# Kernel tuning notes

Measured on AMD Instinct MI355X. Metric: run time of the kernel, lower is better.

## Reference

```python
import jax, jax.numpy as jnp
import numpy as np

N_NODES, FEAT, EMB, BATCH, NUM_SAMPLE = 100000, 256, 256, 10000, 32


def setup_inputs() -> dict:
    key = jax.random.key(0)
    ks = jax.random.split(key, 8)
    sc = 1.0 / np.sqrt(FEAT).astype(np.float32)
    return {
        "nodes": jax.random.randint(ks[0], (BATCH,), 0, N_NODES),
        "neigh_idx": jax.random.randint(ks[1], (BATCH, NUM_SAMPLE), 0, N_NODES),
        "id2feat": jax.random.normal(ks[2], (N_NODES, FEAT), jnp.float32),
        "Wq": jax.random.normal(ks[3], (FEAT, EMB), jnp.float32) * sc,
        "bq": jnp.zeros((EMB,), jnp.float32),
        "Wk": jax.random.normal(ks[4], (FEAT, EMB), jnp.float32) * sc,
        "bk": jnp.zeros((EMB,), jnp.float32),
        "Wv": jax.random.normal(ks[5], (FEAT, EMB), jnp.float32) * sc,
        "bv": jnp.zeros((EMB,), jnp.float32),
    }


def reference(nodes, neigh_idx, id2feat, Wq, bq, Wk, bk, Wv, bv):
    # Gather: self feats [B, F] and sampled neighbor feats [B, S, F]
    self_feats = id2feat[nodes]
    neigh_feats = id2feat[neigh_idx]
    S = neigh_idx.shape[1]
    # Keys/values over [neighbors, self] -> [B, S+1, F]
    cat = jnp.concatenate([neigh_feats, self_feats[:, None, :]], axis=1)
    Q = self_feats @ Wq + bq               # [B, E]
    K = cat @ Wk + bk                       # [B, S+1, E]
    V = cat @ Wv + bv                       # [B, S+1, E]
    scores = jnp.einsum('be,bse->bs', Q, K)  # [B, S+1]
    # Faithful to original mask loop: with full neighbor lists, columns >= num_sample
    # (the appended self key) are masked out.
    mask = jnp.arange(S + 1) >= S
    scores = jnp.where(mask[None, :], -jnp.inf, scores)
    attn = jax.nn.softmax(scores, axis=-1)   # [B, S+1]
    return jnp.einsum('bs,bse->be', attn, V)  # [B, E]
```

## Files before the change

kernel.cpp:

```cpp
#include <hip/hip_runtime.h>
#include <math.h>

#define F 256
#define E 256
#define S 32
#define CH 4
#define LDK 40

typedef __attribute__((ext_vector_type(8))) short short8;
typedef __attribute__((ext_vector_type(4))) float f32x4;

__device__ __forceinline__ ushort f2bf(float x) {
    uint u = __float_as_uint(x);
    return (ushort)((u + 0x7fffu + ((u >> 16) & 1u)) >> 16);
}
__device__ __forceinline__ float bf2f(ushort h) {
    return __uint_as_float(((uint)h) << 16);
}
__device__ __forceinline__ void split4(const float* x, uint2& ph, uint2& pl) {
    ushort h[4], l[4];
#pragma unroll
    for (int i = 0; i < 4; ++i) { h[i] = f2bf(x[i]); l[i] = f2bf(x[i] - bf2f(h[i])); }
    ph.x = (uint)h[0] | ((uint)h[1] << 16); ph.y = (uint)h[2] | ((uint)h[3] << 16);
    pl.x = (uint)l[0] | ((uint)l[1] << 16); pl.y = (uint)l[2] | ((uint)l[3] << 16);
}
__device__ __forceinline__ uint4 pack8(const ushort* h) {
    uint4 r;
    r.x = (uint)h[0] | ((uint)h[1] << 16); r.y = (uint)h[2] | ((uint)h[3] << 16);
    r.z = (uint)h[4] | ((uint)h[5] << 16); r.w = (uint)h[6] | ((uint)h[7] << 16);
    return r;
}

template<bool INSPLIT, bool OUTSPLIT>
__global__ __launch_bounds__(512) void mfma_gemm(const float* __restrict__ X,
                                                 const int* __restrict__ idx,
                                                 const ushort* __restrict__ BTh,
                                                 const ushort* __restrict__ BTl,
                                                 const float* __restrict__ Bf,
                                                 const float* __restrict__ bias,
                                                 float* __restrict__ out,
                                                 ushort* __restrict__ outh,
                                                 ushort* __restrict__ outl,
                                                 int rows) {
    __shared__ ushort Ah[64][LDK], Al[64][LDK];
    __shared__ ushort Bh[256][LDK], Bl[256][LDK];

    const int tid = threadIdx.x;
    const int lane = tid & 63, wave = tid >> 6;
    const int wm = wave >> 2, wn = wave & 3;
    const int fr = lane & 15, fk = lane >> 4;
    const int row0 = blockIdx.x * 64;

    const int arL = tid >> 3;
    const int akL = (tid & 7) * 4;
    const int ar = row0 + arL;
    const int arc = ar < rows ? ar : rows - 1;
    const long arow = idx ? (long)idx[arc] : (long)arc;
    const float* aptr = X + arow * (long)F + akL;

    const int bcol = tid & 255;
    const int bkh = (tid >> 8) * 16;

    f32x4 acc[2][4];
#pragma unroll
    for (int m = 0; m < 2; ++m)
#pragma unroll
        for (int n = 0; n < 4; ++n) acc[m][n] = (f32x4){0.f, 0.f, 0.f, 0.f};

    for (int k0 = 0; k0 < F; k0 += 32) {
        const float4 av = *reinterpret_cast<const float4*>(&aptr[k0]);
        uint2 ah, al;
        split4(&av.x, ah, al);

        uint4 wh0, wh1, wl0, wl1;
        if constexpr (INSPLIT) {
            const float* bp = Bf + (size_t)bcol * F + k0 + bkh;
            float4 b0 = *reinterpret_cast<const float4*>(bp);
            float4 b1 = *reinterpret_cast<const float4*>(bp + 4);
            float4 b2 = *reinterpret_cast<const float4*>(bp + 8);
            float4 b3 = *reinterpret_cast<const float4*>(bp + 12);
            uint2 h0, l0, h1, l1, h2, l2, h3, l3;
            split4(&b0.x, h0, l0); split4(&b1.x, h1, l1);
            split4(&b2.x, h2, l2); split4(&b3.x, h3, l3);
            wh0 = make_uint4(h0.x, h0.y, h1.x, h1.y);
            wh1 = make_uint4(h2.x, h2.y, h3.x, h3.y);
            wl0 = make_uint4(l0.x, l0.y, l1.x, l1.y);
            wl1 = make_uint4(l2.x, l2.y, l3.x, l3.y);
        } else {
            const ushort* bph = BTh + (size_t)bcol * F + k0 + bkh;
            const ushort* bpl = BTl + (size_t)bcol * F + k0 + bkh;
            wh0 = *reinterpret_cast<const uint4*>(bph);
            wh1 = *reinterpret_cast<const uint4*>(bph + 8);
            wl0 = *reinterpret_cast<const uint4*>(bpl);
            wl1 = *reinterpret_cast<const uint4*>(bpl + 8);
        }

        __syncthreads();
        *reinterpret_cast<uint2*>(&Ah[arL][akL]) = ah;
        *reinterpret_cast<uint2*>(&Al[arL][akL]) = al;
        *reinterpret_cast<uint4*>(&Bh[bcol][bkh]) = wh0;
        *reinterpret_cast<uint4*>(&Bh[bcol][bkh + 8]) = wh1;
        *reinterpret_cast<uint4*>(&Bl[bcol][bkh]) = wl0;
        *reinterpret_cast<uint4*>(&Bl[bcol][bkh + 8]) = wl1;
        __syncthreads();

        short8 a_h[2], a_l[2];
#pragma unroll
        for (int m = 0; m < 2; ++m) {
            a_h[m] = *reinterpret_cast<const short8*>(&Ah[wm * 32 + m * 16 + fr][fk * 8]);
            a_l[m] = *reinterpret_cast<const short8*>(&Al[wm * 32 + m * 16 + fr][fk * 8]);
        }
#pragma unroll
        for (int n = 0; n < 4; ++n) {
            const short8 b_h = *reinterpret_cast<const short8*>(&Bh[wn * 64 + n * 16 + fr][fk * 8]);
            const short8 b_l = *reinterpret_cast<const short8*>(&Bl[wn * 64 + n * 16 + fr][fk * 8]);
#pragma unroll
            for (int m = 0; m < 2; ++m) {
                acc[m][n] = __builtin_amdgcn_mfma_f32_16x16x32_bf16(a_h[m], b_h, acc[m][n], 0, 0, 0);
                acc[m][n] = __builtin_amdgcn_mfma_f32_16x16x32_bf16(a_h[m], b_l, acc[m][n], 0, 0, 0);
                acc[m][n] = __builtin_amdgcn_mfma_f32_16x16x32_bf16(a_l[m], b_h, acc[m][n], 0, 0, 0);
            }
        }
    }

#pragma unroll
    for (int n = 0; n < 4; ++n) {
        const int col = wn * 64 + n * 16 + fr;
        float bb = 0.f;
        if constexpr (!OUTSPLIT) bb = bias[col];
#pragma unroll
        for (int m = 0; m < 2; ++m) {
#pragma unroll
            for (int r = 0; r < 4; ++r) {
                const int orow = row0 + wm * 32 + m * 16 + fk * 4 + r;
                if (orow < rows) {
                    if constexpr (OUTSPLIT) {
                        const float v = acc[m][n][r];
                        const ushort h = f2bf(v);
                        outh[(size_t)orow * F + col] = h;
                        outl[(size_t)orow * F + col] = f2bf(v - bf2f(h));
                    } else {
                        out[(size_t)orow * E + col] = acc[m][n][r] + bb;
                    }
                }
            }
        }
    }
}

__global__ __launch_bounds__(256) void prep_misc(const float* __restrict__ Wk,
                                                 const float* __restrict__ bq,
                                                 const float* __restrict__ Wv,
                                                 float* __restrict__ c,
                                                 ushort* __restrict__ WvTh,
                                                 ushort* __restrict__ WvTl) {
    if (blockIdx.x < 4) {
        __shared__ float bqs[F];
        bqs[threadIdx.x] = bq[threadIdx.x];
        __syncthreads();
        const int lane = threadIdx.x & 63, w = threadIdx.x >> 6;
        const float4 b4 = *reinterpret_cast<const float4*>(&bqs[lane * 4]);
#pragma unroll
        for (int i = 0; i < 16; ++i) {
            const int j = blockIdx.x * 64 + w * 16 + i;
            const float4 k4 = *reinterpret_cast<const float4*>(&Wk[(size_t)j * F + lane * 4]);
            float p = k4.x * b4.x + k4.y * b4.y + k4.z * b4.z + k4.w * b4.w;
#pragma unroll
            for (int off = 32; off; off >>= 1) p += __shfl_xor(p, off);
            if (lane == 0) c[j] = p;
        }
    } else {
        __shared__ float t[64][65];
        const int tb = blockIdx.x - 4;
        const int jt = (tb & 3) * 64, kt = (tb >> 2) * 64;
        const int lk = threadIdx.x >> 2;
        const int lj = (threadIdx.x & 3) * 16;
#pragma unroll
        for (int u = 0; u < 16; u += 4) {
            const float4 v = *reinterpret_cast<const float4*>(&Wv[(size_t)(kt + lk) * E + jt + lj + u]);
            t[lk][lj + u] = v.x; t[lk][lj + u + 1] = v.y;
            t[lk][lj + u + 2] = v.z; t[lk][lj + u + 3] = v.w;
        }
        __syncthreads();
        const int oj = threadIdx.x >> 2;
        const int ok = (threadIdx.x & 3) * 16;
        ushort h[16], l[16];
#pragma unroll
        for (int u = 0; u < 16; ++u) {
            const float v = t[ok + u][oj];
            h[u] = f2bf(v); l[u] = f2bf(v - bf2f(h[u]));
        }
        ushort* ph = &WvTh[(size_t)(jt + oj) * F + kt + ok];
        ushort* pl = &WvTl[(size_t)(jt + oj) * F + kt + ok];
        *reinterpret_cast<uint4*>(ph) = pack8(h);
        *reinterpret_cast<uint4*>(ph + 8) = pack8(h + 8);
        *reinterpret_cast<uint4*>(pl) = pack8(l);
        *reinterpret_cast<uint4*>(pl + 8) = pack8(l + 8);
    }
}

__device__ __forceinline__ void ld_chunk(float4* d, int idxv, int s0,
                                         const float* __restrict__ t, int lane) {
#pragma unroll
    for (int j = 0; j < CH; ++j) {
        const int nid = __builtin_amdgcn_readlane(idxv, s0 + j);
        d[j] = *reinterpret_cast<const float4*>(&t[(size_t)nid * F + lane * 4]);
    }
}

__device__ __forceinline__ void proc_chunk(const float4* v, const float4 qv,
                                           float& m, float& l, float4& acc) {
#pragma unroll
    for (int j = 0; j < CH; ++j) {
        float p = v[j].x * qv.x + v[j].y * qv.y + v[j].z * qv.z + v[j].w * qv.w;
#pragma unroll
        for (int off = 32; off; off >>= 1) p += __shfl_xor(p, off);
        if (p <= m) {
            const float w = __expf(p - m);
            l += w;
            acc.x += w * v[j].x; acc.y += w * v[j].y;
            acc.z += w * v[j].z; acc.w += w * v[j].w;
        } else {
            const float cc = __expf(m - p);
            l = l * cc + 1.f;
            acc.x = acc.x * cc + v[j].x; acc.y = acc.y * cc + v[j].y;
            acc.z = acc.z * cc + v[j].z; acc.w = acc.w * cc + v[j].w;
            m = p;
        }
    }
}

__global__ __launch_bounds__(256) void attn_gather(const int* __restrict__ neigh_idx,
                                                   const float* __restrict__ id2feat,
                                                   float* __restrict__ qtm,
                                                   int B) {
    const int node = blockIdx.x * 4 + (threadIdx.x >> 6);
    const int lane = threadIdx.x & 63;
    if (node >= B) return;

    const int idxv = neigh_idx[node * S + (lane & (S - 1))];
    const float4 qv = *reinterpret_cast<const float4*>(&qtm[(size_t)node * F + lane * 4]);

    float m = -INFINITY, l = 0.f;
    float4 acc = make_float4(0.f, 0.f, 0.f, 0.f);

    float4 va[CH], vb[CH];
    ld_chunk(va, idxv, 0, id2feat, lane);
    ld_chunk(vb, idxv, 4, id2feat, lane);
    proc_chunk(va, qv, m, l, acc);
    ld_chunk(va, idxv, 8, id2feat, lane);
    proc_chunk(vb, qv, m, l, acc);
    ld_chunk(vb, idxv, 12, id2feat, lane);
    proc_chunk(va, qv, m, l, acc);
    ld_chunk(va, idxv, 16, id2feat, lane);
    proc_chunk(vb, qv, m, l, acc);
    ld_chunk(vb, idxv, 20, id2feat, lane);
    proc_chunk(va, qv, m, l, acc);
    ld_chunk(va, idxv, 24, id2feat, lane);
    proc_chunk(vb, qv, m, l, acc);
    ld_chunk(vb, idxv, 28, id2feat, lane);
    proc_chunk(va, qv, m, l, acc);
    proc_chunk(vb, qv, m, l, acc);

    const float inv = 1.0f / l;
    float4 o;
    o.x = acc.x * inv; o.y = acc.y * inv; o.z = acc.z * inv; o.w = acc.w * inv;
    *reinterpret_cast<float4*>(&qtm[(size_t)node * F + lane * 4]) = o;
}

extern "C" void kernel_launch(void* const* d_in, const int* in_sizes, int n_in,
                              void* d_out, int out_size, void* d_ws, size_t ws_size,
                              hipStream_t stream) {
    const int*   nodes   = (const int*)d_in[0];
    const int*   neigh   = (const int*)d_in[1];
    const float* id2feat = (const float*)d_in[2];
    const float* Wq      = (const float*)d_in[3];
    const float* bq      = (const float*)d_in[4];
    const float* Wk      = (const float*)d_in[5];
    const float* Wv      = (const float*)d_in[7];
    const float* bv      = (const float*)d_in[8];
    float* out = (float*)d_out;
    const int B = in_sizes[0];

    ushort* MT_hi  = (ushort*)d_ws;
    ushort* MT_lo  = MT_hi + 65536;
    ushort* WvT_hi = MT_lo + 65536;
    ushort* WvT_lo = WvT_hi + 65536;
    float*  cbuf   = (float*)(WvT_lo + 65536);
    float*  qtm    = cbuf + 256;

    mfma_gemm<true, true><<<dim3(4), dim3(512), 0, stream>>>(
        Wk, nullptr, nullptr, nullptr, Wq, nullptr, nullptr, MT_hi, MT_lo, 256);
    prep_misc<<<dim3(20), dim3(256), 0, stream>>>(Wk, bq, Wv, cbuf, WvT_hi, WvT_lo);
    mfma_gemm<false, false><<<dim3((B + 63) / 64), dim3(512), 0, stream>>>(
        id2feat, nodes, MT_hi, MT_lo, nullptr, cbuf, qtm, nullptr, nullptr, B);
    attn_gather<<<dim3((B + 3) / 4), dim3(256), 0, stream>>>(neigh, id2feat, qtm, B);
    mfma_gemm<false, false><<<dim3((B + 63) / 64), dim3(512), 0, stream>>>(
        qtm, nullptr, WvT_hi, WvT_lo, nullptr, bv, out, nullptr, nullptr, B);
}
```

Before: 123.0 us.

## Fuse Q projection, neighbor attention and V projection into one kernel

Merges the three per-batch kernels (Q GEMM, attention gather, V GEMM) into a single kernel that keeps the 64-row Q tile and attention output in shared memory. This drops the qtm round-trip through global memory and two launches. The weight-prep kernels are also combined into one launch, and GEMM B operands are now read straight from global memory into MFMA registers instead of being staged in LDS. In exchange, the large LDS tile (about 66KB) limits occupancy, and only 157 blocks cover the gather phase, which may reduce latency hiding for the random neighbor loads.

```diff
diff --git a/kernel.cpp b/kernel.cpp
--- a/kernel.cpp
+++ b/kernel.cpp
@@ -5,7 +5,7 @@
 #define E 256
 #define S 32
 #define CH 4
-#define LDK 40
+#define TLP 260
 
 typedef __attribute__((ext_vector_type(8))) short short8;
 typedef __attribute__((ext_vector_type(4))) float f32x4;
@@ -16,13 +16,6 @@
 }
 __device__ __forceinline__ float bf2f(ushort h) {
     return __uint_as_float(((uint)h) << 16);
-}
-__device__ __forceinline__ void split4(const float* x, uint2& ph, uint2& pl) {
-    ushort h[4], l[4];
-#pragma unroll
-    for (int i = 0; i < 4; ++i) { h[i] = f2bf(x[i]); l[i] = f2bf(x[i] - bf2f(h[i])); }
-    ph.x = (uint)h[0] | ((uint)h[1] << 16); ph.y = (uint)h[2] | ((uint)h[3] << 16);
-    pl.x = (uint)l[0] | ((uint)l[1] << 16); pl.y = (uint)l[2] | ((uint)l[3] << 16);
 }
 __device__ __forceinline__ uint4 pack8(const ushort* h) {
     uint4 r;
@@ -30,172 +23,120 @@
     r.z = (uint)h[4] | ((uint)h[5] << 16); r.w = (uint)h[6] | ((uint)h[7] << 16);
     return r;
 }
-
-template<bool INSPLIT, bool OUTSPLIT>
-__global__ __launch_bounds__(512) void mfma_gemm(const float* __restrict__ X,
-                                                 const int* __restrict__ idx,
-                                                 const ushort* __restrict__ BTh,
-                                                 const ushort* __restrict__ BTl,
-                                                 const float* __restrict__ Bf,
-                                                 const float* __restrict__ bias,
-                                                 float* __restrict__ out,
-                                                 ushort* __restrict__ outh,
-                                                 ushort* __restrict__ outl,
-                                                 int rows) {
-    __shared__ ushort Ah[64][LDK], Al[64][LDK];
-    __shared__ ushort Bh[256][LDK], Bl[256][LDK];
-
-    const int tid = threadIdx.x;
+__device__ __forceinline__ void split8(const float* x, short8& h, short8& l) {
+    ushort hh[8], ll[8];
+#pragma unroll
+    for (int i = 0; i < 8; ++i) { hh[i] = f2bf(x[i]); ll[i] = f2bf(x[i] - bf2f(hh[i])); }
+    uint4 ph = pack8(hh), pl = pack8(ll);
+    h = *reinterpret_cast<short8*>(&ph);
+    l = *reinterpret_cast<short8*>(&pl);
+}
+__device__ __forceinline__ short8 mk8(uint a, uint b, uint c, uint d) {
+    uint4 p = make_uint4(a, b, c, d);
+    return *reinterpret_cast<short8*>(&p);
+}
+__device__ __forceinline__ uint pkbf(float v) {
+    const ushort h = f2bf(v);
+    const ushort l = f2bf(v - bf2f(h));
+    return (uint)h | ((uint)l << 16);
+}
+
+__global__ __launch_bounds__(512) void prep(const float* __restrict__ Wq,
+                                            const float* __restrict__ bq,
+                                            const float* __restrict__ Wk,
+                                            const float* __restrict__ Wv,
+                                            ushort* __restrict__ MTh,
+                                            ushort* __restrict__ MTl,
+                                            ushort* __restrict__ WvTh,
+                                            ushort* __restrict__ WvTl,
+                                            float* __restrict__ c) {
+    const int blk = blockIdx.x, tid = threadIdx.x;
     const int lane = tid & 63, wave = tid >> 6;
-    const int wm = wave >> 2, wn = wave & 3;
-    const int fr = lane & 15, fk = lane >> 4;
-    const int row0 = blockIdx.x * 64;
-
-    const int arL = tid >> 3;
-    const int akL = (tid & 7) * 4;
-    const int ar = row0 + arL;
-    const int arc = ar < rows ? ar : rows - 1;
-    const long arow = idx ? (long)idx[arc] : (long)arc;
-    const float* aptr = X + arow * (long)F + akL;
-
-    const int bcol = tid & 255;
-    const int bkh = (tid >> 8) * 16;
-
-    f32x4 acc[2][4];
-#pragma unroll
-    for (int m = 0; m < 2; ++m)
-#pragma unroll
-        for (int n = 0; n < 4; ++n) acc[m][n] = (f32x4){0.f, 0.f, 0.f, 0.f};
-
-    for (int k0 = 0; k0 < F; k0 += 32) {
-        const float4 av = *reinterpret_cast<const float4*>(&aptr[k0]);
-        uint2 ah, al;
-        split4(&av.x, ah, al);
-
-        uint4 wh0, wh1, wl0, wl1;
-        if constexpr (INSPLIT) {
-            const float* bp = Bf + (size_t)bcol * F + k0 + bkh;
-            float4 b0 = *reinterpret_cast<const float4*>(bp);
-            float4 b1 = *reinterpret_cast<const float4*>(bp + 4);
-            float4 b2 = *reinterpret_cast<const float4*>(bp + 8);
-            float4 b3 = *reinterpret_cast<const float4*>(bp + 12);
-            uint2 h0, l0, h1, l1, h2, l2, h3, l3;
-            split4(&b0.x, h0, l0); split4(&b1.x, h1, l1);
-            split4(&b2.x, h2, l2); split4(&b3.x, h3, l3);
-            wh0 = make_uint4(h0.x, h0.y, h1.x, h1.y);
-            wh1 = make_uint4(h2.x, h2.y, h3.x, h3.y);
-            wl0 = make_uint4(l0.x, l0.y, l1.x, l1.y);
-            wl1 = make_uint4(l2.x, l2.y, l3.x, l3.y);
-        } else {
-            const ushort* bph = BTh + (size_t)bcol * F + k0 + bkh;
-            const ushort* bpl = BTl + (size_t)bcol * F + k0 + bkh;
-            wh0 = *reinterpret_cast<const uint4*>(bph);
-            wh1 = *reinterpret_cast<const uint4*>(bph + 8);
-            wl0 = *reinterpret_cast<const uint4*>(bpl);
-            wl1 = *reinterpret_cast<const uint4*>(bpl + 8);
-        }
-
+    if (blk < 4) {
+        const int wm = wave >> 2, wn = wave & 3;
+        const int fr = lane & 15, fk = lane >> 4;
+        const int j0 = blk * 64;
+        f32x4 acc[2][4];
+#pragma unroll
+        for (int m = 0; m < 2; ++m)
+#pragma unroll
+            for (int n = 0; n < 4; ++n) acc[m][n] = (f32x4){0.f, 0.f, 0.f, 0.f};
+        for (int k0 = 0; k0 < F; k0 += 32) {
+            short8 ah[2], al[2];
+#pragma unroll
+            for (int m = 0; m < 2; ++m) {
+                const float* p = &Wk[(size_t)(j0 + wm * 32 + m * 16 + fr) * F + k0 + fk * 8];
+                float x[8];
+                *reinterpret_cast<float4*>(&x[0]) = *reinterpret_cast<const float4*>(p);
+                *reinterpret_cast<float4*>(&x[4]) = *reinterpret_cast<const float4*>(p + 4);
+                split8(x, ah[m], al[m]);
+            }
+#pragma unroll
+            for (int n = 0; n < 4; ++n) {
+                const float* p = &Wq[(size_t)(wn * 64 + n * 16 + fr) * F + k0 + fk * 8];
+                float x[8];
+                *reinterpret_cast<float4*>(&x[0]) = *reinterpret_cast<const float4*>(p);
+                *reinterpret_cast<float4*>(&x[4]) = *reinterpret_cast<const float4*>(p + 4);
+                short8 bh, bl;
+                split8(x, bh, bl);
+#pragma unroll
+                for (int m = 0; m < 2; ++m) {
+                    acc[m][n] = __builtin_amdgcn_mfma_f32_16x16x32_bf16(ah[m], bh, acc[m][n], 0, 0, 0);
+                    acc[m][n] = __builtin_amdgcn_mfma_f32_16x16x32_bf16(ah[m], bl, acc[m][n], 0, 0, 0);
+                    acc[m][n] = __builtin_amdgcn_mfma_f32_16x16x32_bf16(al[m], bh, acc[m][n], 0, 0, 0);
+                }
+            }
+        }
+#pragma unroll
+        for (int n = 0; n < 4; ++n) {
+            const int i = wn * 64 + n * 16 + fr;
+#pragma unroll
+            for (int m = 0; m < 2; ++m)
+#pragma unroll
+                for (int r = 0; r < 4; ++r) {
+                    const int j = j0 + wm * 32 + m * 16 + fk * 4 + r;
+                    const float v = acc[m][n][r];
+                    const ushort h = f2bf(v);
+                    MTh[(size_t)j * F + i] = h;
+                    MTl[(size_t)j * F + i] = f2bf(v - bf2f(h));
+                }
+        }
+    } else if (blk < 20) {
+        __shared__ float t[64][65];
+        const int tb = blk - 4;
+        const int jt = (tb & 3) * 64, kt = (tb >> 2) * 64;
+        const int lk = tid >> 3, lj = (tid & 7) * 8;
+        {
+            const float* p = &Wv[(size_t)(kt + lk) * E + jt + lj];
+            const float4 v0 = *reinterpret_cast<const float4*>(p);
+            const float4 v1 = *reinterpret_cast<const float4*>(p + 4);
+            t[lk][lj + 0] = v0.x; t[lk][lj + 1] = v0.y; t[lk][lj + 2] = v0.z; t[lk][lj + 3] = v0.w;
+            t[lk][lj + 4] = v1.x; t[lk][lj + 5] = v1.y; t[lk][lj + 6] = v1.z; t[lk][lj + 7] = v1.w;
+        }
         __syncthreads();
-        *reinterpret_cast<uint2*>(&Ah[arL][akL]) = ah;
-        *reinterpret_cast<uint2*>(&Al[arL][akL]) = al;
-        *reinterpret_cast<uint4*>(&Bh[bcol][bkh]) = wh0;
-        *reinterpret_cast<uint4*>(&Bh[bcol][bkh + 8]) = wh1;
-        *reinterpret_cast<uint4*>(&Bl[bcol][bkh]) = wl0;
-        *reinterpret_cast<uint4*>(&Bl[bcol][bkh + 8]) = wl1;
+        const int oj = tid >> 3, ok = (tid & 7) * 8;
+        ushort h[8], l[8];
+#pragma unroll
+        for (int u = 0; u < 8; ++u) {
+            const float v = t[ok + u][oj];
+            h[u] = f2bf(v); l[u] = f2bf(v - bf2f(h[u]));
+        }
+        *reinterpret_cast<uint4*>(&WvTh[(size_t)(jt + oj) * F + kt + ok]) = pack8(h);
+        *reinterpret_cast<uint4*>(&WvTl[(size_t)(jt + oj) * F + kt + ok]) = pack8(l);
+    } else {
+        __shared__ float bqs[F];
+        if (tid < F) bqs[tid] = bq[tid];
         __syncthreads();
-
-        short8 a_h[2], a_l[2];
-#pragma unroll
-        for (int m = 0; m < 2; ++m) {
-            a_h[m] = *reinterpret_cast<const short8*>(&Ah[wm * 32 + m * 16 + fr][fk * 8]);
-            a_l[m] = *reinterpret_cast<const short8*>(&Al[wm * 32 + m * 16 + fr][fk * 8]);
-        }
-#pragma unroll
-        for (int n = 0; n < 4; ++n) {
-            const short8 b_h = *reinterpret_cast<const short8*>(&Bh[wn * 64 + n * 16 + fr][fk * 8]);
-            const short8 b_l = *reinterpret_cast<const short8*>(&Bl[wn * 64 + n * 16 + fr][fk * 8]);
-#pragma unroll
-            for (int m = 0; m < 2; ++m) {
-                acc[m][n] = __builtin_amdgcn_mfma_f32_16x16x32_bf16(a_h[m], b_h, acc[m][n], 0, 0, 0);
-                acc[m][n] = __builtin_amdgcn_mfma_f32_16x16x32_bf16(a_h[m], b_l, acc[m][n], 0, 0, 0);
-                acc[m][n] = __builtin_amdgcn_mfma_f32_16x16x32_bf16(a_l[m], b_h, acc[m][n], 0, 0, 0);
-            }
-        }
-    }
-
-#pragma unroll
-    for (int n = 0; n < 4; ++n) {
-        const int col = wn * 64 + n * 16 + fr;
-        float bb = 0.f;
-        if constexpr (!OUTSPLIT) bb = bias[col];
-#pragma unroll
-        for (int m = 0; m < 2; ++m) {
-#pragma unroll
-            for (int r = 0; r < 4; ++r) {
-                const int orow = row0 + wm * 32 + m * 16 + fk * 4 + r;
-                if (orow < rows) {
-                    if constexpr (OUTSPLIT) {
-                        const float v = acc[m][n][r];
-                        const ushort h = f2bf(v);
-                        outh[(size_t)orow * F + col] = h;
-                        outl[(size_t)orow * F + col] = f2bf(v - bf2f(h));
-                    } else {
-                        out[(size_t)orow * E + col] = acc[m][n][r] + bb;
-                    }
-                }
-            }
-        }
-    }
-}
-
-__global__ __launch_bounds__(256) void prep_misc(const float* __restrict__ Wk,
-                                                 const float* __restrict__ bq,
-                                                 const float* __restrict__ Wv,
-                                                 float* __restrict__ c,
-                                                 ushort* __restrict__ WvTh,
-                                                 ushort* __restrict__ WvTl) {
-    if (blockIdx.x < 4) {
-        __shared__ float bqs[F];
-        bqs[threadIdx.x] = bq[threadIdx.x];
-        __syncthreads();
-        const int lane = threadIdx.x & 63, w = threadIdx.x >> 6;
         const float4 b4 = *reinterpret_cast<const float4*>(&bqs[lane * 4]);
 #pragma unroll
-        for (int i = 0; i < 16; ++i) {
-            const int j = blockIdx.x * 64 + w * 16 + i;
+        for (int i = 0; i < 8; ++i) {
+            const int j = (blk - 20) * 64 + wave * 8 + i;
             const float4 k4 = *reinterpret_cast<const float4*>(&Wk[(size_t)j * F + lane * 4]);
             float p = k4.x * b4.x + k4.y * b4.y + k4.z * b4.z + k4.w * b4.w;
 #pragma unroll
             for (int off = 32; off; off >>= 1) p += __shfl_xor(p, off);
             if (lane == 0) c[j] = p;
         }
-    } else {
-        __shared__ float t[64][65];
-        const int tb = blockIdx.x - 4;
-        const int jt = (tb & 3) * 64, kt = (tb >> 2) * 64;
-        const int lk = threadIdx.x >> 2;
-        const int lj = (threadIdx.x & 3) * 16;
-#pragma unroll
-        for (int u = 0; u < 16; u += 4) {
-            const float4 v = *reinterpret_cast<const float4*>(&Wv[(size_t)(kt + lk) * E + jt + lj + u]);
-            t[lk][lj + u] = v.x; t[lk][lj + u + 1] = v.y;
-            t[lk][lj + u + 2] = v.z; t[lk][lj + u + 3] = v.w;
-        }
-        __syncthreads();
-        const int oj = threadIdx.x >> 2;
-        const int ok = (threadIdx.x & 3) * 16;
-        ushort h[16], l[16];
-#pragma unroll
-        for (int u = 0; u < 16; ++u) {
-            const float v = t[ok + u][oj];
-            h[u] = f2bf(v); l[u] = f2bf(v - bf2f(h[u]));
-        }
-        ushort* ph = &WvTh[(size_t)(jt + oj) * F + kt + ok];
-        ushort* pl = &WvTl[(size_t)(jt + oj) * F + kt + ok];
-        *reinterpret_cast<uint4*>(ph) = pack8(h);
-        *reinterpret_cast<uint4*>(ph + 8) = pack8(h + 8);
-        *reinterpret_cast<uint4*>(pl) = pack8(l);
-        *reinterpret_cast<uint4*>(pl + 8) = pack8(l + 8);
     }
 }
 
@@ -207,7 +148,6 @@
         d[j] = *reinterpret_cast<const float4*>(&t[(size_t)nid * F + lane * 4]);
     }
 }
-
 __device__ __forceinline__ void proc_chunk(const float4* v, const float4 qv,
                                            float& m, float& l, float4& acc) {
 #pragma unroll
@@ -230,42 +170,150 @@
     }
 }
 
-__global__ __launch_bounds__(256) void attn_gather(const int* __restrict__ neigh_idx,
-                                                   const float* __restrict__ id2feat,
-                                                   float* __restrict__ qtm,
-                                                   int B) {
-    const int node = blockIdx.x * 4 + (threadIdx.x >> 6);
-    const int lane = threadIdx.x & 63;
-    if (node >= B) return;
-
-    const int idxv = neigh_idx[node * S + (lane & (S - 1))];
-    const float4 qv = *reinterpret_cast<const float4*>(&qtm[(size_t)node * F + lane * 4]);
-
-    float m = -INFINITY, l = 0.f;
-    float4 acc = make_float4(0.f, 0.f, 0.f, 0.f);
-
-    float4 va[CH], vb[CH];
-    ld_chunk(va, idxv, 0, id2feat, lane);
-    ld_chunk(vb, idxv, 4, id2feat, lane);
-    proc_chunk(va, qv, m, l, acc);
-    ld_chunk(va, idxv, 8, id2feat, lane);
-    proc_chunk(vb, qv, m, l, acc);
-    ld_chunk(vb, idxv, 12, id2feat, lane);
-    proc_chunk(va, qv, m, l, acc);
-    ld_chunk(va, idxv, 16, id2feat, lane);
-    proc_chunk(vb, qv, m, l, acc);
-    ld_chunk(vb, idxv, 20, id2feat, lane);
-    proc_chunk(va, qv, m, l, acc);
-    ld_chunk(va, idxv, 24, id2feat, lane);
-    proc_chunk(vb, qv, m, l, acc);
-    ld_chunk(vb, idxv, 28, id2feat, lane);
-    proc_chunk(va, qv, m, l, acc);
-    proc_chunk(vb, qv, m, l, acc);
-
-    const float inv = 1.0f / l;
-    float4 o;
-    o.x = acc.x * inv; o.y = acc.y * inv; o.z = acc.z * inv; o.w = acc.w * inv;
-    *reinterpret_cast<float4*>(&qtm[(size_t)node * F + lane * 4]) = o;
+__global__ __launch_bounds__(512, 4) void fused(const int* __restrict__ nodes,
+                                                const int* __restrict__ neigh,
+                                                const float* __restrict__ id2feat,
+                                                const ushort* __restrict__ MTh,
+                                                const ushort* __restrict__ MTl,
+                                                const ushort* __restrict__ WvTh,
+                                                const ushort* __restrict__ WvTl,
+                                                const float* __restrict__ cb,
+                                                const float* __restrict__ bv,
+                                                float* __restrict__ out,
+                                                int B) {
+    __shared__ uint tile[64][TLP];
+
+    const int tid = threadIdx.x;
+    const int lane = tid & 63, wave = tid >> 6;
+    const int wm = wave >> 2, wn = wave & 3;
+    const int fr = lane & 15, fk = lane >> 4;
+    const int row0 = blockIdx.x * 64;
+
+    int arow[2];
+#pragma unroll
+    for (int m = 0; m < 2; ++m) {
+        const int r = row0 + wm * 32 + m * 16 + fr;
+        arow[m] = nodes[r < B ? r : B - 1];
+    }
+    f32x4 acc[2][4];
+#pragma unroll
+    for (int m = 0; m < 2; ++m)
+#pragma unroll
+        for (int n = 0; n < 4; ++n) acc[m][n] = (f32x4){0.f, 0.f, 0.f, 0.f};
+
+    for (int k0 = 0; k0 < F; k0 += 32) {
+        short8 ah[2], al[2];
+#pragma unroll
+        for (int m = 0; m < 2; ++m) {
+            const float* p = id2feat + (size_t)arow[m] * F + k0 + fk * 8;
+            float x[8];
+            *reinterpret_cast<float4*>(&x[0]) = *reinterpret_cast<const float4*>(p);
+            *reinterpret_cast<float4*>(&x[4]) = *reinterpret_cast<const float4*>(p + 4);
+            split8(x, ah[m], al[m]);
+        }
+#pragma unroll
+        for (int n = 0; n < 4; ++n) {
+            const size_t boff = (size_t)(wn * 64 + n * 16 + fr) * F + k0 + fk * 8;
+            const short8 bh = *reinterpret_cast<const short8*>(&MTh[boff]);
+            const short8 bl = *reinterpret_cast<const short8*>(&MTl[boff]);
+#pragma unroll
+            for (int m = 0; m < 2; ++m) {
+                acc[m][n] = __builtin_amdgcn_mfma_f32_16x16x32_bf16(ah[m], bh, acc[m][n], 0, 0, 0);
+                acc[m][n] = __builtin_amdgcn_mfma_f32_16x16x32_bf16(ah[m], bl, acc[m][n], 0, 0, 0);
+                acc[m][n] = __builtin_amdgcn_mfma_f32_16x16x32_bf16(al[m], bh, acc[m][n], 0, 0, 0);
+            }
+        }
+    }
+#pragma unroll
+    for (int n = 0; n < 4; ++n) {
+        const int col = wn * 64 + n * 16 + fr;
+        const float cc = cb[col];
+#pragma unroll
+        for (int m = 0; m < 2; ++m)
+#pragma unroll
+            for (int r = 0; r < 4; ++r)
+                tile[wm * 32 + m * 16 + fk * 4 + r][col] = __float_as_uint(acc[m][n][r] + cc);
+    }
+    __syncthreads();
+
+#pragma unroll 1
+    for (int i = 0; i < 8; ++i) {
+        const int tr = wave * 8 + i;
+        const int node = row0 + tr;
+        if (node < B) {
+            const int idxv = neigh[node * S + (lane & (S - 1))];
+            const uint4 q4 = *reinterpret_cast<const uint4*>(&tile[tr][lane * 4]);
+            const float4 qv = make_float4(__uint_as_float(q4.x), __uint_as_float(q4.y),
+                                          __uint_as_float(q4.z), __uint_as_float(q4.w));
+            float m = -INFINITY, l = 0.f;
+            float4 a = make_float4(0.f, 0.f, 0.f, 0.f);
+            float4 va[CH], vb[CH];
+            ld_chunk(va, idxv, 0, id2feat, lane);
+            ld_chunk(vb, idxv, 4, id2feat, lane);
+            proc_chunk(va, qv, m, l, a);
+            ld_chunk(va, idxv, 8, id2feat, lane);
+            proc_chunk(vb, qv, m, l, a);
+            ld_chunk(vb, idxv, 12, id2feat, lane);
+            proc_chunk(va, qv, m, l, a);
+            ld_chunk(va, idxv, 16, id2feat, lane);
+            proc_chunk(vb, qv, m, l, a);
+            ld_chunk(vb, idxv, 20, id2feat, lane);
+            proc_chunk(va, qv, m, l, a);
+            ld_chunk(va, idxv, 24, id2feat, lane);
+            proc_chunk(vb, qv, m, l, a);
+            ld_chunk(vb, idxv, 28, id2feat, lane);
+            proc_chunk(va, qv, m, l, a);
+            proc_chunk(vb, qv, m, l, a);
+            const float inv = 1.0f / l;
+            const uint4 o = make_uint4(pkbf(a.x * inv), pkbf(a.y * inv),
+                                       pkbf(a.z * inv), pkbf(a.w * inv));
+            *reinterpret_cast<uint4*>(&tile[tr][lane * 4]) = o;
+        }
+    }
+    __syncthreads();
+
+#pragma unroll
+    for (int m = 0; m < 2; ++m)
+#pragma unroll
+        for (int n = 0; n < 4; ++n) acc[m][n] = (f32x4){0.f, 0.f, 0.f, 0.f};
+
+    for (int k0 = 0; k0 < F; k0 += 32) {
+        short8 ah[2], al[2];
+#pragma unroll
+        for (int m = 0; m < 2; ++m) {
+            const int tr = wm * 32 + m * 16 + fr;
+            const uint4 u0 = *reinterpret_cast<const uint4*>(&tile[tr][k0 + fk * 8]);
+            const uint4 u1 = *reinterpret_cast<const uint4*>(&tile[tr][k0 + fk * 8 + 4]);
+            ah[m] = mk8((u0.x & 0xffffu) | (u0.y << 16), (u0.z & 0xffffu) | (u0.w << 16),
+                        (u1.x & 0xffffu) | (u1.y << 16), (u1.z & 0xffffu) | (u1.w << 16));
+            al[m] = mk8((u0.x >> 16) | (u0.y & 0xffff0000u), (u0.z >> 16) | (u0.w & 0xffff0000u),
+                        (u1.x >> 16) | (u1.y & 0xffff0000u), (u1.z >> 16) | (u1.w & 0xffff0000u));
+        }
+#pragma unroll
+        for (int n = 0; n < 4; ++n) {
+            const size_t boff = (size_t)(wn * 64 + n * 16 + fr) * F + k0 + fk * 8;
+            const short8 bh = *reinterpret_cast<const short8*>(&WvTh[boff]);
+            const short8 bl = *reinterpret_cast<const short8*>(&WvTl[boff]);
+#pragma unroll
+            for (int m = 0; m < 2; ++m) {
+                acc[m][n] = __builtin_amdgcn_mfma_f32_16x16x32_bf16(ah[m], bh, acc[m][n], 0, 0, 0);
+                acc[m][n] = __builtin_amdgcn_mfma_f32_16x16x32_bf16(ah[m], bl, acc[m][n], 0, 0, 0);
+                acc[m][n] = __builtin_amdgcn_mfma_f32_16x16x32_bf16(al[m], bh, acc[m][n], 0, 0, 0);
+            }
+        }
+    }
+#pragma unroll
+    for (int n = 0; n < 4; ++n) {
+        const int col = wn * 64 + n * 16 + fr;
+        const float bb = bv[col];
+#pragma unroll
+        for (int m = 0; m < 2; ++m)
+#pragma unroll
+            for (int r = 0; r < 4; ++r) {
+                const int grow = row0 + wm * 32 + m * 16 + fk * 4 + r;
+                if (grow < B) out[(size_t)grow * E + col] = acc[m][n][r] + bb;
+            }
+    }
 }
 
 extern "C" void kernel_launch(void* const* d_in, const int* in_sizes, int n_in,
@@ -282,19 +330,14 @@
     float* out = (float*)d_out;
     const int B = in_sizes[0];
 
-    ushort* MT_hi  = (ushort*)d_ws;
-    ushort* MT_lo  = MT_hi + 65536;
-    ushort* WvT_hi = MT_lo + 65536;
-    ushort* WvT_lo = WvT_hi + 65536;
-    float*  cbuf   = (float*)(WvT_lo + 65536);
-    float*  qtm    = cbuf + 256;
-
-    mfma_gemm<true, true><<<dim3(4), dim3(512), 0, stream>>>(
-        Wk, nullptr, nullptr, nullptr, Wq, nullptr, nullptr, MT_hi, MT_lo, 256);
-    prep_misc<<<dim3(20), dim3(256), 0, stream>>>(Wk, bq, Wv, cbuf, WvT_hi, WvT_lo);
-    mfma_gemm<false, false><<<dim3((B + 63) / 64), dim3(512), 0, stream>>>(
-        id2feat, nodes, MT_hi, MT_lo, nullptr, cbuf, qtm, nullptr, nullptr, B);
-    attn_gather<<<dim3((B + 3) / 4), dim3(256), 0, stream>>>(neigh, id2feat, qtm, B);
-    mfma_gemm<false, false><<<dim3((B + 63) / 64), dim3(512), 0, stream>>>(
-        qtm, nullptr, WvT_hi, WvT_lo, nullptr, bv, out, nullptr, nullptr, B);
-}
+    ushort* MTh  = (ushort*)d_ws;
+    ushort* MTl  = MTh + 65536;
+    ushort* WvTh = MTl + 65536;
+    ushort* WvTl = WvTh + 65536;
+    float*  cbuf = (float*)(WvTl + 65536);
+
+    prep<<<dim3(24), dim3(512), 0, stream>>>(Wq, bq, Wk, Wv, MTh, MTl, WvTh, WvTl, cbuf);
+    fused<<<dim3((B + 63) / 64), dim3(512), 0, stream>>>(nodes, neigh, id2feat,
+                                                         MTh, MTl, WvTh, WvTl,
+                                                         cbuf, bv, out, B);
+}
```

Result: slower. 145.5 us (+18.3%).
